# Kernel optimization log

Measured on AMD Instinct MI355X. Metric: run time of the kernel, lower is better.

Reference implementation:

```python
import jax, jax.numpy as jnp
import numpy as np


def setup_inputs() -> dict:
    key = jax.random.key(0)
    k0, k1, k2, k3 = jax.random.split(key, 4)
    B, T, M, E, H = 4, 2048, 1024, 8, 4096
    x = jax.random.normal(k0, (B, T, M), dtype=jnp.float32)
    wg = jax.random.normal(k1, (M, E), dtype=jnp.float32) * 0.02
    w1 = jax.random.normal(k2, (E, M, H), dtype=jnp.float32) * 0.02
    w2 = jax.random.normal(k3, (E, H, M), dtype=jnp.float32) * 0.02
    return {"x": x, "wg": wg, "w1": w1, "w2": w2}


def reference(x, wg, w1, w2):
    """GShard MoE layer: top-1 gate + dense one-hot dispatch/combine + expert FFN."""
    M = x.shape[-1]
    xs = x.reshape(-1, M)                      # [s, m]
    s = xs.shape[0]
    E = wg.shape[1]
    capacity = s // E                          # capacity_factor = 1.0

    # ---- top-1 gate (deepspeed/gshard top1gating) ----
    logits = xs @ wg                           # [s, e]
    gates = jax.nn.softmax(logits, axis=-1)
    idx = jnp.argmax(gates, axis=1)            # [s]
    mask1 = jax.nn.one_hot(idx, E, dtype=gates.dtype)  # [s, e]
    me = gates.mean(axis=0)
    ce = mask1.mean(axis=0)
    l_aux = jnp.sum(me * ce) * E
    # position of each token within its expert's buffer
    locations = jnp.cumsum(mask1, axis=0) - 1.0          # [s, e]
    mask1 = mask1 * (locations < capacity).astype(gates.dtype)  # drop overflow
    gates1 = gates * mask1                                 # [s, e]
    loc_s = jnp.sum(locations * mask1, axis=1).astype(jnp.int32)  # [s]
    loc_sc = jax.nn.one_hot(loc_s, capacity, dtype=gates.dtype)   # [s, c]
    combine = gates1[:, :, None] * loc_sc[:, None, :]       # [s, e, c]
    dispatch = (combine > 0).astype(x.dtype)                # [s, e, c]

    # ---- dense one-hot dispatch (the kernel-headroom hotspot) ----
    dispatched = jnp.einsum('sec,sm->ecm', dispatch, xs)    # [e, c, m]

    # ---- per-expert 2-layer FFN ----
    h = jax.nn.relu(jnp.einsum('ecm,emh->ech', dispatched, w1))
    expert_out = jnp.einsum('ech,ehm->ecm', h, w2)          # [e, c, m]

    # ---- dense one-hot combine ----
    out = jnp.einsum('sec,ecm->sm', combine, expert_out).reshape(x.shape)
    return out, l_aux
```

## Files before the change

kernel.cpp:

```cpp
#include <hip/hip_runtime.h>
#include <hip/hip_bf16.h>

#define S_TOK 8192
#define MDIM  1024
#define EXP   8
#define HDIM  4096
#define CAP   1024

typedef __attribute__((ext_vector_type(8))) short short8;
typedef __attribute__((ext_vector_type(4))) float floatx4;

__device__ __forceinline__ unsigned short f2b(float f) {
    union { float f; unsigned int i; } v; v.f = f;
    unsigned int r = v.i + 0x7fffu + ((v.i >> 16) & 1u);
    return (unsigned short)(r >> 16);
}

__device__ __forceinline__ void gl2lds16(const unsigned short* g, unsigned short* l) {
    __builtin_amdgcn_global_load_lds(
        (const __attribute__((address_space(1))) unsigned int*)g,
        (__attribute__((address_space(3))) unsigned int*)l,
        16, 0, 0);
}

__global__ __launch_bounds__(256) void gate_kernel(
    const float* __restrict__ x, const float* __restrict__ wg,
    float* __restrict__ gates8, int* __restrict__ token_expert)
{
    const int wave = threadIdx.x >> 6, lane = threadIdx.x & 63;
    const int s = blockIdx.x * 4 + wave;

    const float* xr = x + (size_t)s * MDIM + lane * 16;
    float xv[16];
#pragma unroll
    for (int q = 0; q < 4; ++q) *(float4*)(xv + q * 4) = *(const float4*)(xr + q * 4);

    float acc[EXP];
#pragma unroll
    for (int e = 0; e < EXP; ++e) acc[e] = 0.f;
    const int m0 = lane * 16;
#pragma unroll
    for (int j = 0; j < 16; ++j) {
        const float xm = xv[j];
        const float* wr = wg + (size_t)(m0 + j) * EXP;
        float4 w0 = *(const float4*)(wr);
        float4 w1v = *(const float4*)(wr + 4);
        acc[0] += xm * w0.x; acc[1] += xm * w0.y; acc[2] += xm * w0.z; acc[3] += xm * w0.w;
        acc[4] += xm * w1v.x; acc[5] += xm * w1v.y; acc[6] += xm * w1v.z; acc[7] += xm * w1v.w;
    }
#pragma unroll
    for (int e = 0; e < EXP; ++e) {
#pragma unroll
        for (int off = 32; off > 0; off >>= 1)
            acc[e] += __shfl_down(acc[e], off);
    }
    if (lane == 0) {
        float mx = acc[0]; int idx = 0;
#pragma unroll
        for (int e = 1; e < EXP; ++e) if (acc[e] > mx) { mx = acc[e]; idx = e; }
        float g[EXP]; float sum = 0.f;
#pragma unroll
        for (int e = 0; e < EXP; ++e) { g[e] = expf(acc[e] - mx); sum += g[e]; }
        float inv = 1.f / sum;
#pragma unroll
        for (int e = 0; e < EXP; ++e) gates8[(size_t)s * EXP + e] = g[e] * inv;
        token_expert[s] = idx;
    }
}

__global__ __launch_bounds__(256) void scan_kernel(
    const float* __restrict__ gates8, const int* __restrict__ token_expert,
    int* __restrict__ slot_token, float* __restrict__ slot_gate,
    float* __restrict__ laux_out)
{
    __shared__ int   cnt[256][EXP];
    __shared__ float fsum[256][EXP];
    __shared__ int   tot[EXP];
    const int t = threadIdx.x;

    for (int i = t; i < EXP * CAP; i += 256) slot_token[i] = -1;

    int local[EXP];
#pragma unroll
    for (int e = 0; e < EXP; ++e) local[e] = 0;
    const int s0 = t * 32;
    for (int j = 0; j < 32; ++j) local[token_expert[s0 + j]]++;
#pragma unroll
    for (int e = 0; e < EXP; ++e) cnt[t][e] = local[e];
    __syncthreads();

    if (t < EXP) {
        int run = 0;
        for (int i = 0; i < 256; ++i) { int v = cnt[i][t]; cnt[i][t] = run; run += v; }
        tot[t] = run;
    }
    __syncthreads();

    int off[EXP];
#pragma unroll
    for (int e = 0; e < EXP; ++e) off[e] = cnt[t][e];
    for (int j = 0; j < 32; ++j) {
        int s = s0 + j;
        int e = token_expert[s];
        int loc = off[e]++;
        if (loc < CAP) {
            int slot = e * CAP + loc;
            slot_token[slot] = s;
            slot_gate[slot]  = gates8[(size_t)s * EXP + e];
        }
    }

    float ms[EXP];
#pragma unroll
    for (int e = 0; e < EXP; ++e) ms[e] = 0.f;
    for (int j = 0; j < 32; ++j) {
        const float* g = gates8 + (size_t)(s0 + j) * EXP;
#pragma unroll
        for (int e = 0; e < EXP; ++e) ms[e] += g[e];
    }
#pragma unroll
    for (int e = 0; e < EXP; ++e) fsum[t][e] = ms[e];
    __syncthreads();
    for (int st = 128; st > 0; st >>= 1) {
        if (t < st) {
#pragma unroll
            for (int e = 0; e < EXP; ++e) fsum[t][e] += fsum[t + st][e];
        }
        __syncthreads();
    }
    if (t == 0) {
        float l = 0.f;
#pragma unroll
        for (int e = 0; e < EXP; ++e)
            l += (fsum[0][e] / (float)S_TOK) * ((float)tot[e] / (float)S_TOK);
        laux_out[0] = l * (float)EXP;
    }
}

__global__ __launch_bounds__(256) void dispatch_cvt(
    const float* __restrict__ x, const int* __restrict__ slot_token,
    unsigned short* __restrict__ xd)
{
    const int slot = blockIdx.x, t = threadIdx.x;
    const int tok = slot_token[slot];
    unsigned short v[4];
    if (tok >= 0) {
        float4 f = *(const float4*)(x + (size_t)tok * MDIM + t * 4);
        v[0] = f2b(f.x); v[1] = f2b(f.y); v[2] = f2b(f.z); v[3] = f2b(f.w);
    } else {
        v[0] = v[1] = v[2] = v[3] = 0;
    }
    *(int2*)(xd + (size_t)slot * MDIM + t * 4) = *(const int2*)v;
}

__global__ __launch_bounds__(256) void transpose_cvt(
    const float* __restrict__ src, unsigned short* __restrict__ dst, int R, int C)
{
    __shared__ unsigned short Ls[64 * 72];
    const size_t eo = (size_t)blockIdx.z * R * C;
    src += eo; dst += eo;
    const int C0 = blockIdx.x * 64, R0 = blockIdx.y * 64;
    const int t = threadIdx.x;
    {
        const int r = t >> 2, c0 = (t & 3) * 16;
        const float* p = src + (size_t)(R0 + r) * C + C0 + c0;
        float f[16];
#pragma unroll
        for (int q = 0; q < 4; ++q) *(float4*)(f + q * 4) = ((const float4*)p)[q];
#pragma unroll
        for (int j = 0; j < 16; ++j) Ls[(c0 + j) * 72 + r] = f2b(f[j]);
    }
    __syncthreads();
    {
        const int c = t >> 2, m0 = (t & 3) * 16;
        int4 v0 = *(const int4*)&Ls[c * 72 + m0];
        int4 v1 = *(const int4*)&Ls[c * 72 + m0 + 8];
        int4* q = (int4*)(dst + (size_t)(C0 + c) * R + R0 + m0);
        q[0] = v0; q[1] = v1;
    }
}

template<int KSTEPS, int N, bool SCATTER>
__global__ __launch_bounds__(256) void ffn_gemm_fast(
    const unsigned short* __restrict__ Ab, const unsigned short* __restrict__ BT,
    void* __restrict__ Outv,
    const int* __restrict__ slot_token, const float* __restrict__ slot_gate)
{
    constexpr int K = KSTEPS * 32;
    const int e  = blockIdx.z;
    const int ib = blockIdx.y * 128;
    const int nb = blockIdx.x * 128;
    const int t  = threadIdx.x;

    __shared__ unsigned short As[2][128 * 32];
    __shared__ unsigned short Bs[2][128 * 32];

    const int lane = t & 63, wave = t >> 6;
    const int quad = lane >> 4, l15 = lane & 15;
    const int wr = wave >> 1, wc = wave & 1;

    const int c0    = wave * 2;
    const int srow  = lane >> 2;
    const int kpart = (lane & 3) * 8;

    const unsigned short* Ag = Ab + (size_t)(e * CAP + ib) * K + kpart;
    const unsigned short* Bg = BT + ((size_t)e * N + nb) * K + kpart;
    const size_t row0 = (size_t)(c0 * 16 + srow) * K;
    const size_t row1 = (size_t)(c0 * 16 + 16 + srow) * K;

    floatx4 acc[4][4];
#pragma unroll
    for (int r = 0; r < 4; ++r)
#pragma unroll
        for (int c = 0; c < 4; ++c)
            acc[r][c] = (floatx4){0.f, 0.f, 0.f, 0.f};

    auto stage = [&](int buf, int kb) {
        const int k0 = kb * 32;
        gl2lds16(Ag + row0 + k0, &As[buf][(c0    ) * 512]);
        gl2lds16(Ag + row1 + k0, &As[buf][(c0 + 1) * 512]);
        gl2lds16(Bg + row0 + k0, &Bs[buf][(c0    ) * 512]);
        gl2lds16(Bg + row1 + k0, &Bs[buf][(c0 + 1) * 512]);
    };

    int cur = 0;
    stage(0, 0);
    __syncthreads();

    for (int kb = 0; kb < KSTEPS; ++kb) {
        if (kb + 1 < KSTEPS) stage(cur ^ 1, kb + 1);

        short8 af[4], bfr[4];
#pragma unroll
        for (int r = 0; r < 4; ++r)
            af[r] = *(const short8*)&As[cur][(wr * 64 + r * 16 + l15) * 32 + quad * 8];
#pragma unroll
        for (int c = 0; c < 4; ++c)
            bfr[c] = *(const short8*)&Bs[cur][(wc * 64 + c * 16 + l15) * 32 + quad * 8];
#pragma unroll
        for (int r = 0; r < 4; ++r)
#pragma unroll
            for (int c = 0; c < 4; ++c)
                acc[r][c] = __builtin_amdgcn_mfma_f32_16x16x32_bf16(af[r], bfr[c], acc[r][c], 0, 0, 0);

        __syncthreads();
        cur ^= 1;
    }

#pragma unroll
    for (int r = 0; r < 4; ++r) {
#pragma unroll
        for (int reg = 0; reg < 4; ++reg) {
            const int gi = ib + wr * 64 + r * 16 + quad * 4 + reg;
            if (SCATTER) {
                const int slot = e * CAP + gi;
                const int tok = slot_token[slot];
                if (tok >= 0) {
                    const float gsc = slot_gate[slot];
                    float* Out = (float*)Outv;
#pragma unroll
                    for (int c = 0; c < 4; ++c) {
                        const int gn = nb + wc * 64 + c * 16 + l15;
                        Out[(size_t)tok * N + gn] = gsc * acc[r][c][reg];
                    }
                }
            } else {
                unsigned short* Out = (unsigned short*)Outv;
#pragma unroll
                for (int c = 0; c < 4; ++c) {
                    const int gn = nb + wc * 64 + c * 16 + l15;
                    Out[((size_t)e * CAP + gi) * N + gn] = f2b(fmaxf(acc[r][c][reg], 0.f));
                }
            }
        }
    }
}

template<int KSTEPS, int N, bool GATHER, bool SCATTER>
__global__ __launch_bounds__(256) void ffn_gemm_slow(
    const void* __restrict__ Agv, const float* __restrict__ Bg,
    void* __restrict__ Outv,
    const int* __restrict__ slot_token, const float* __restrict__ slot_gate)
{
    constexpr int K = KSTEPS * 32;
    const int e  = blockIdx.z;
    const int ib = blockIdx.y * 128;
    const int nb = blockIdx.x * 128;
    const int t  = threadIdx.x;

    __shared__ unsigned short As[128 * 40];
    __shared__ unsigned short Bs[32 * 136];

    const float* B = Bg + (size_t)e * K * N;
    const int arow  = t >> 1;
    const int ahalf = t & 1;
    const float* ArowF = nullptr;
    const unsigned short* ArowH = nullptr;
    bool avalid = true;
    if (GATHER) {
        int tok = slot_token[e * CAP + ib + arow];
        avalid = (tok >= 0);
        ArowF = (const float*)Agv + (size_t)(avalid ? tok : 0) * K;
    } else {
        ArowH = (const unsigned short*)Agv + ((size_t)e * CAP + ib + arow) * K;
    }
    const int bk  = t >> 3;
    const int bn0 = (t & 7) * 16;
    const float* Bptr = B + (size_t)bk * N + nb + bn0;

    const int lane = t & 63, wave = t >> 6;
    const int quad = lane >> 4, l15 = lane & 15;
    const int wr = wave >> 1, wc = wave & 1;

    floatx4 acc[4][4];
#pragma unroll
    for (int r = 0; r < 4; ++r)
#pragma unroll
        for (int c = 0; c < 4; ++c)
            acc[r][c] = (floatx4){0.f, 0.f, 0.f, 0.f};

    for (int kb = 0; kb < KSTEPS; ++kb) {
        const int k0 = kb * 32;
        unsigned short av[16];
        if (GATHER) {
            if (avalid) {
                const float4* p = (const float4*)(ArowF + k0 + ahalf * 16);
                float4 f0 = p[0], f1 = p[1], f2 = p[2], f3 = p[3];
                const float fa[16] = {f0.x,f0.y,f0.z,f0.w, f1.x,f1.y,f1.z,f1.w,
                                      f2.x,f2.y,f2.z,f2.w, f3.x,f3.y,f3.z,f3.w};
#pragma unroll
                for (int j = 0; j < 16; ++j) av[j] = f2b(fa[j]);
            } else {
#pragma unroll
                for (int j = 0; j < 16; ++j) av[j] = 0;
            }
        } else {
            const int4* p = (const int4*)(ArowH + k0 + ahalf * 16);
            *(int4*)(av)     = p[0];
            *(int4*)(av + 8) = p[1];
        }
        unsigned short bv[16];
        {
            const float4* q = (const float4*)(Bptr + (size_t)k0 * N);
            float4 f0 = q[0], f1 = q[1], f2 = q[2], f3 = q[3];
            const float fb[16] = {f0.x,f0.y,f0.z,f0.w, f1.x,f1.y,f1.z,f1.w,
                                  f2.x,f2.y,f2.z,f2.w, f3.x,f3.y,f3.z,f3.w};
#pragma unroll
            for (int j = 0; j < 16; ++j) bv[j] = f2b(fb[j]);
        }

        *(int4*)&As[arow * 40 + ahalf * 16]     = *(int4*)(av);
        *(int4*)&As[arow * 40 + ahalf * 16 + 8] = *(int4*)(av + 8);
        *(int4*)&Bs[bk * 136 + bn0]             = *(int4*)(bv);
        *(int4*)&Bs[bk * 136 + bn0 + 8]         = *(int4*)(bv + 8);
        __syncthreads();

        short8 af[4];
#pragma unroll
        for (int r = 0; r < 4; ++r)
            af[r] = *(const short8*)&As[(wr * 64 + r * 16 + l15) * 40 + quad * 8];
        short8 bfr[4];
#pragma unroll
        for (int c = 0; c < 4; ++c) {
#pragma unroll
            for (int j = 0; j < 8; ++j)
                bfr[c][j] = (short)Bs[(quad * 8 + j) * 136 + wc * 64 + c * 16 + l15];
        }
#pragma unroll
        for (int r = 0; r < 4; ++r)
#pragma unroll
            for (int c = 0; c < 4; ++c)
                acc[r][c] = __builtin_amdgcn_mfma_f32_16x16x32_bf16(af[r], bfr[c], acc[r][c], 0, 0, 0);
        __syncthreads();
    }

#pragma unroll
    for (int r = 0; r < 4; ++r) {
#pragma unroll
        for (int reg = 0; reg < 4; ++reg) {
            const int gi = ib + wr * 64 + r * 16 + quad * 4 + reg;
            if (SCATTER) {
                const int slot = e * CAP + gi;
                const int tok = slot_token[slot];
                if (tok >= 0) {
                    const float gsc = slot_gate[slot];
                    float* Out = (float*)Outv;
#pragma unroll
                    for (int c = 0; c < 4; ++c) {
                        const int gn = nb + wc * 64 + c * 16 + l15;
                        Out[(size_t)tok * N + gn] = gsc * acc[r][c][reg];
                    }
                }
            } else {
                unsigned short* Out = (unsigned short*)Outv;
#pragma unroll
                for (int c = 0; c < 4; ++c) {
                    const int gn = nb + wc * 64 + c * 16 + l15;
                    Out[((size_t)e * CAP + gi) * N + gn] = f2b(fmaxf(acc[r][c][reg], 0.f));
                }
            }
        }
    }
}

extern "C" void kernel_launch(void* const* d_in, const int* in_sizes, int n_in,
                              void* d_out, int out_size, void* d_ws, size_t ws_size,
                              hipStream_t stream)
{
    const float* x  = (const float*)d_in[0];
    const float* wg = (const float*)d_in[1];
    const float* w1 = (const float*)d_in[2];
    const float* w2 = (const float*)d_in[3];
    float* out = (float*)d_out;

    char* ws = (char*)d_ws;
    float* gates8       = (float*)(ws);
    int*   token_expert = (int*)(ws + 262144);
    int*   slot_token   = (int*)(ws + 294912);
    float* slot_gate    = (float*)(ws + 327680);

    hipMemsetAsync(d_out, 0, (size_t)out_size * 4, stream);
    gate_kernel<<<dim3(S_TOK / 4), dim3(256), 0, stream>>>(x, wg, gates8, token_expert);
    scan_kernel<<<dim3(1), dim3(256), 0, stream>>>(gates8, token_expert, slot_token, slot_gate,
                                                   out + (size_t)S_TOK * MDIM);

    const size_t FAST_NEED = 151355392ull;
    if (ws_size >= FAST_NEED) {
        unsigned short* xd = (unsigned short*)(ws + 360448);
        unsigned short* h  = (unsigned short*)(ws + 17137664);
        unsigned short* W  = (unsigned short*)(ws + 84246528);

        dispatch_cvt<<<dim3(EXP * CAP), dim3(256), 0, stream>>>(x, slot_token, xd);
        transpose_cvt<<<dim3(HDIM / 64, MDIM / 64, EXP), dim3(256), 0, stream>>>(w1, W, MDIM, HDIM);
        ffn_gemm_fast<32, HDIM, false><<<dim3(HDIM / 128, CAP / 128, EXP), dim3(256), 0, stream>>>(
            xd, W, h, slot_token, slot_gate);
        transpose_cvt<<<dim3(MDIM / 64, HDIM / 64, EXP), dim3(256), 0, stream>>>(w2, W, HDIM, MDIM);
        ffn_gemm_fast<128, MDIM, true><<<dim3(MDIM / 128, CAP / 128, EXP), dim3(256), 0, stream>>>(
            h, W, out, slot_token, slot_gate);
    } else {
        unsigned short* h = (unsigned short*)(ws + 360448);
        ffn_gemm_slow<32, HDIM, true, false><<<dim3(HDIM / 128, CAP / 128, EXP), dim3(256), 0, stream>>>(
            x, w1, h, slot_token, slot_gate);
        ffn_gemm_slow<128, MDIM, false, true><<<dim3(MDIM / 128, CAP / 128, EXP), dim3(256), 0, stream>>>(
            h, w2, out, slot_token, slot_gate);
    }
}
```

Baseline: 622.3 us.

## Add 8-wave 256x128 triple-buffered MFMA GEMM with interleaved LDS staging

Adds a new expert FFN GEMM kernel that uses 512-thread workgroups computing 256x128 output tiles with a 64-wide K step. It triple-buffers A and B tiles in dynamic LDS (144 KB) via direct global-to-LDS loads, and splits those loads into slices interleaved between MFMA phases. Explicit vmcnt waits, barriers, sched_barrier and setprio shape the schedule. It also remaps workgroup ids across XCDs for cache locality. The aim is more MFMA throughput and better load/compute overlap than the 128x128 double-buffered kernel, at the cost of one workgroup per CU and a fallback path if the large LDS request fails.

```diff
diff --git a/kernel.cpp b/kernel.cpp
--- a/kernel.cpp
+++ b/kernel.cpp
@@ -9,6 +9,11 @@
 
 typedef __attribute__((ext_vector_type(8))) short short8;
 typedef __attribute__((ext_vector_type(4))) float floatx4;
+
+#define BARRIER() asm volatile("s_barrier" ::: "memory")
+#define WAITV6()  asm volatile("s_waitcnt vmcnt(6)" ::: "memory")
+#define WAITV0()  asm volatile("s_waitcnt vmcnt(0)" ::: "memory")
+#define SCHEDB()  __builtin_amdgcn_sched_barrier(0)
 
 __device__ __forceinline__ unsigned short f2b(float f) {
     union { float f; unsigned int i; } v; v.f = f;
@@ -177,6 +182,171 @@
         int4 v1 = *(const int4*)&Ls[c * 72 + m0 + 8];
         int4* q = (int4*)(dst + (size_t)(C0 + c) * R + R0 + m0);
         q[0] = v0; q[1] = v1;
+    }
+}
+
+template<int KT, int N, bool SCATTER>
+__global__ __launch_bounds__(512, 2) void ffn_gemm_8p(
+    const unsigned short* __restrict__ Ag, const unsigned short* __restrict__ BT,
+    void* __restrict__ Outv,
+    const int* __restrict__ slot_token, const float* __restrict__ slot_gate)
+{
+    constexpr int K   = KT * 64;
+    constexpr int NBX = N / 128;
+    constexpr int NWG = NBX * (CAP / 256);
+
+    extern __shared__ __align__(16) unsigned short sm[];
+    unsigned short* Abuf = sm;
+    unsigned short* Bbuf = sm + 3 * 16384;
+
+    const int e    = blockIdx.z;
+    const int orig = blockIdx.x;
+    const int logical = (orig & 7) * (NWG >> 3) + (orig >> 3);
+    const int nb = (logical % NBX) * 128;
+    const int ib = (logical / NBX) * 256;
+
+    const int tid  = threadIdx.x;
+    const int lane = tid & 63, wave = tid >> 6;
+    const int quad = lane >> 4, l15 = lane & 15;
+    const int wm = wave >> 2, wn = wave & 3;
+
+    const int rr   = tid >> 3;
+    const int slot = (tid & 7) ^ (rr & 7);
+    const unsigned short* Asrc = Ag + (size_t)(e * CAP + ib + rr) * K + slot * 8;
+    const unsigned short* Bsrc = BT + ((size_t)e * N + nb + rr) * K + slot * 8;
+
+    auto stageA = [&](int buf, int t, int ca) {
+        gl2lds16(Asrc + (size_t)ca * 64 * K + t * 64,
+                 Abuf + buf * 16384 + ca * 4096 + wave * 512);
+    };
+    auto stageB = [&](int buf, int t, int cb) {
+        gl2lds16(Bsrc + (size_t)cb * 64 * K + t * 64,
+                 Bbuf + buf * 8192 + cb * 4096 + wave * 512);
+    };
+
+    const int sx  = l15 & 7;
+    const int ko0 = ((0 + quad) ^ sx) * 8;
+    const int ko1 = ((4 + quad) ^ sx) * 8;
+    const int arow = wm * 128 + l15;
+    const int brow = wn * 32 + l15;
+
+    floatx4 acc[8][2];
+#pragma unroll
+    for (int i = 0; i < 8; ++i)
+#pragma unroll
+        for (int j = 0; j < 2; ++j)
+            acc[i][j] = (floatx4){0.f, 0.f, 0.f, 0.f};
+
+#pragma unroll
+    for (int ca = 0; ca < 4; ++ca) stageA(0, 0, ca);
+#pragma unroll
+    for (int cb = 0; cb < 2; ++cb) stageB(0, 0, cb);
+#pragma unroll
+    for (int ca = 0; ca < 4; ++ca) stageA(1, 1, ca);
+#pragma unroll
+    for (int cb = 0; cb < 2; ++cb) stageB(1, 1, cb);
+    WAITV6();
+    BARRIER();
+
+    int buf = 0;
+    for (int t = 0; t < KT; ++t) {
+        const int nbuf = (buf >= 1) ? buf - 1 : 2;
+        const bool st  = (t + 2 < KT);
+
+        short8 brg[2][2];
+#pragma unroll
+        for (int fn = 0; fn < 2; ++fn) {
+            const int row = brow + fn * 16;
+            brg[fn][0] = *(const short8*)&Bbuf[buf * 8192 + row * 64 + ko0];
+            brg[fn][1] = *(const short8*)&Bbuf[buf * 8192 + row * 64 + ko1];
+        }
+        short8 aA[8];
+#pragma unroll
+        for (int fm = 0; fm < 4; ++fm) {
+            const int row = arow + fm * 16;
+            aA[fm * 2 + 0] = *(const short8*)&Abuf[buf * 16384 + row * 64 + ko0];
+            aA[fm * 2 + 1] = *(const short8*)&Abuf[buf * 16384 + row * 64 + ko1];
+        }
+        if (st) { stageA(nbuf, t + 2, 0); stageA(nbuf, t + 2, 1); }
+        BARRIER(); SCHEDB();
+        __builtin_amdgcn_s_setprio(1);
+#pragma unroll
+        for (int fm = 0; fm < 4; ++fm) {
+            acc[fm][0] = __builtin_amdgcn_mfma_f32_16x16x32_bf16(aA[fm*2+0], brg[0][0], acc[fm][0], 0, 0, 0);
+            acc[fm][0] = __builtin_amdgcn_mfma_f32_16x16x32_bf16(aA[fm*2+1], brg[0][1], acc[fm][0], 0, 0, 0);
+        }
+        __builtin_amdgcn_s_setprio(0); SCHEDB(); BARRIER();
+
+        short8 aB[8];
+#pragma unroll
+        for (int fm = 0; fm < 4; ++fm) {
+            const int row = arow + 64 + fm * 16;
+            aB[fm * 2 + 0] = *(const short8*)&Abuf[buf * 16384 + row * 64 + ko0];
+            aB[fm * 2 + 1] = *(const short8*)&Abuf[buf * 16384 + row * 64 + ko1];
+        }
+        if (st) { stageA(nbuf, t + 2, 2); stageA(nbuf, t + 2, 3); }
+        BARRIER(); SCHEDB();
+        __builtin_amdgcn_s_setprio(1);
+#pragma unroll
+        for (int fm = 0; fm < 4; ++fm) {
+            acc[fm][1] = __builtin_amdgcn_mfma_f32_16x16x32_bf16(aA[fm*2+0], brg[1][0], acc[fm][1], 0, 0, 0);
+            acc[fm][1] = __builtin_amdgcn_mfma_f32_16x16x32_bf16(aA[fm*2+1], brg[1][1], acc[fm][1], 0, 0, 0);
+        }
+        __builtin_amdgcn_s_setprio(0); SCHEDB(); BARRIER();
+
+        if (st) stageB(nbuf, t + 2, 0);
+        BARRIER(); SCHEDB();
+        __builtin_amdgcn_s_setprio(1);
+#pragma unroll
+        for (int fm = 0; fm < 4; ++fm) {
+            acc[4+fm][0] = __builtin_amdgcn_mfma_f32_16x16x32_bf16(aB[fm*2+0], brg[0][0], acc[4+fm][0], 0, 0, 0);
+            acc[4+fm][0] = __builtin_amdgcn_mfma_f32_16x16x32_bf16(aB[fm*2+1], brg[0][1], acc[4+fm][0], 0, 0, 0);
+        }
+        __builtin_amdgcn_s_setprio(0); SCHEDB(); BARRIER();
+
+        if (st) stageB(nbuf, t + 2, 1);
+        BARRIER(); SCHEDB();
+        __builtin_amdgcn_s_setprio(1);
+#pragma unroll
+        for (int fm = 0; fm < 4; ++fm) {
+            acc[4+fm][1] = __builtin_amdgcn_mfma_f32_16x16x32_bf16(aB[fm*2+0], brg[1][0], acc[4+fm][1], 0, 0, 0);
+            acc[4+fm][1] = __builtin_amdgcn_mfma_f32_16x16x32_bf16(aB[fm*2+1], brg[1][1], acc[4+fm][1], 0, 0, 0);
+        }
+        __builtin_amdgcn_s_setprio(0); SCHEDB();
+        if (t + 1 < KT) {
+            if (st) WAITV6(); else WAITV0();
+            BARRIER();
+        }
+        buf = (buf == 2) ? 0 : buf + 1;
+    }
+
+#pragma unroll
+    for (int FM = 0; FM < 8; ++FM) {
+        const int rowb = ib + wm * 128 + FM * 16 + quad * 4;
+#pragma unroll
+        for (int r = 0; r < 4; ++r) {
+            const int gi = rowb + r;
+            if (SCATTER) {
+                const int slotI = e * CAP + gi;
+                const int tok = slot_token[slotI];
+                if (tok >= 0) {
+                    const float gsc = slot_gate[slotI];
+                    float* Out = (float*)Outv;
+#pragma unroll
+                    for (int fn = 0; fn < 2; ++fn) {
+                        const int gn = nb + wn * 32 + fn * 16 + l15;
+                        Out[(size_t)tok * N + gn] = gsc * acc[FM][fn][r];
+                    }
+                }
+            } else {
+                unsigned short* Out = (unsigned short*)Outv;
+#pragma unroll
+                for (int fn = 0; fn < 2; ++fn) {
+                    const int gn = nb + wn * 32 + fn * 16 + l15;
+                    Out[((size_t)e * CAP + gi) * N + gn] = f2b(fmaxf(acc[FM][fn][r], 0.f));
+                }
+            }
+        }
     }
 }
 
@@ -430,13 +600,32 @@
         unsigned short* h  = (unsigned short*)(ws + 17137664);
         unsigned short* W  = (unsigned short*)(ws + 84246528);
 
+        static bool tried = false, ok8 = false;
+        if (!tried) {
+            tried = true;
+            ok8 = (hipFuncSetAttribute((const void*)ffn_gemm_8p<16, HDIM, false>,
+                       hipFuncAttributeMaxDynamicSharedMemorySize, 147456) == hipSuccess)
+               && (hipFuncSetAttribute((const void*)ffn_gemm_8p<64, MDIM, true>,
+                       hipFuncAttributeMaxDynamicSharedMemorySize, 147456) == hipSuccess);
+        }
+
         dispatch_cvt<<<dim3(EXP * CAP), dim3(256), 0, stream>>>(x, slot_token, xd);
         transpose_cvt<<<dim3(HDIM / 64, MDIM / 64, EXP), dim3(256), 0, stream>>>(w1, W, MDIM, HDIM);
-        ffn_gemm_fast<32, HDIM, false><<<dim3(HDIM / 128, CAP / 128, EXP), dim3(256), 0, stream>>>(
-            xd, W, h, slot_token, slot_gate);
+        if (ok8) {
+            ffn_gemm_8p<16, HDIM, false><<<dim3((HDIM/128) * (CAP/256), 1, EXP), dim3(512), 147456, stream>>>(
+                xd, W, h, slot_token, slot_gate);
+        } else {
+            ffn_gemm_fast<32, HDIM, false><<<dim3(HDIM / 128, CAP / 128, EXP), dim3(256), 0, stream>>>(
+                xd, W, h, slot_token, slot_gate);
+        }
         transpose_cvt<<<dim3(MDIM / 64, HDIM / 64, EXP), dim3(256), 0, stream>>>(w2, W, HDIM, MDIM);
-        ffn_gemm_fast<128, MDIM, true><<<dim3(MDIM / 128, CAP / 128, EXP), dim3(256), 0, stream>>>(
-            h, W, out, slot_token, slot_gate);
+        if (ok8) {
+            ffn_gemm_8p<64, MDIM, true><<<dim3((MDIM/128) * (CAP/256), 1, EXP), dim3(512), 147456, stream>>>(
+                h, W, out, slot_token, slot_gate);
+        } else {
+            ffn_gemm_fast<128, MDIM, true><<<dim3(MDIM / 128, CAP / 128, EXP), dim3(256), 0, stream>>>(
+                h, W, out, slot_token, slot_gate);
+        }
     } else {
         unsigned short* h = (unsigned short*)(ws + 360448);
         ffn_gemm_slow<32, HDIM, true, false><<<dim3(HDIM / 128, CAP / 128, EXP), dim3(256), 0, stream>>>(
```

Result: faster. 568.9 us (-8.6%).
